# Kernel optimization log

Measured on AMD Instinct MI355X. Metric: run time of the kernel, lower is better.

The kernel has to match this reference:

```python
import jax, jax.numpy as jnp
import numpy as np

NUM_NODES = 200000
B = 65536          # n_id batch size
E = 131072         # events per direction
D_MEM = 128
D_RAW = 128
D_TIME = 128
T_MAX = 1000000


def setup_inputs() -> dict:
    key = jax.random.key(0)
    ks = jax.random.split(key, 16)
    inp = {
        'memory': jax.random.normal(ks[0], (NUM_NODES, D_MEM), jnp.float32),
        'last_update': jax.random.randint(ks[1], (NUM_NODES,), 0, 1000, jnp.int64),
        'n_id': jnp.arange(B, dtype=jnp.int64),
        'src_s': jax.random.randint(ks[2], (E,), 0, B, jnp.int64),
        'dst_s': jax.random.randint(ks[3], (E,), 0, B, jnp.int64),
        't_s': jax.random.randint(ks[4], (E,), 0, T_MAX, jnp.int64),
        'raw_msg_s': jax.random.normal(ks[5], (E, D_RAW), jnp.float32),
        'src_d': jax.random.randint(ks[6], (E,), 0, B, jnp.int64),
        'dst_d': jax.random.randint(ks[7], (E,), 0, B, jnp.int64),
        't_d': jax.random.randint(ks[8], (E,), 0, T_MAX, jnp.int64),
        'raw_msg_d': jax.random.normal(ks[9], (E, D_RAW), jnp.float32),
        'w_time': jax.random.normal(ks[10], (D_TIME, 1), jnp.float32) * 0.1,
        'b_time': jax.random.normal(ks[11], (D_TIME,), jnp.float32) * 0.1,
        'W_ih': jax.random.normal(ks[12], (3 * D_MEM, 2 * D_MEM + D_RAW + D_TIME), jnp.float32) * 0.05,
        'W_hh': jax.random.normal(ks[13], (3 * D_MEM, D_MEM), jnp.float32) * 0.05,
        'b_ih': jax.random.normal(ks[14], (3 * D_MEM,), jnp.float32) * 0.05,
        'b_hh': jax.random.normal(ks[15], (3 * D_MEM,), jnp.float32) * 0.05,
    }
    return inp


def _time_enc(t_rel, w_time, b_time):
    # Linear(1, time_dim) followed by cos: cos(t * w + b)
    return jnp.cos(t_rel.astype(jnp.float32)[:, None] * w_time[:, 0][None, :] + b_time)


def reference(memory, last_update, n_id, src_s, dst_s, t_s, raw_msg_s,
              src_d, dst_d, t_d, raw_msg_d, w_time, b_time, W_ih, W_hh, b_ih, b_hh):
    nb = n_id.shape[0]
    # assoc: global node id -> local index within n_id
    assoc = jnp.zeros((memory.shape[0],), dtype=jnp.int32).at[n_id].set(
        jnp.arange(nb, dtype=jnp.int32))

    # source-side messages (IdentityMessage = concat)
    t_enc_s = _time_enc(t_s - last_update[src_s], w_time, b_time)
    msg_s = jnp.concatenate([memory[src_s], memory[dst_s], raw_msg_s, t_enc_s], axis=-1)

    # destination-side messages
    t_enc_d = _time_enc(t_d - last_update[dst_d], w_time, b_time)
    msg_d = jnp.concatenate([memory[dst_d], memory[src_d], raw_msg_d, t_enc_d], axis=-1)

    idx = jnp.concatenate([src_s, dst_d], axis=0)       # [2E] global ids
    msg = jnp.concatenate([msg_s, msg_d], axis=0)       # [2E, 512]
    t = jnp.concatenate([t_s, t_d], axis=0)             # [2E]
    loc = assoc[idx]                                     # [2E] local ids

    # LastAggregator: per local node, pick the message with max t (ties -> latest position)
    ne = t.shape[0]
    key = t * ne + jnp.arange(ne, dtype=t.dtype)         # encode (t, position)
    maxkey = jax.ops.segment_max(key, loc, num_segments=nb)
    count = jax.ops.segment_sum(jnp.ones_like(loc), loc, num_segments=nb)
    has = count > 0
    argm = jnp.where(has, maxkey % ne, 0)
    aggr = jnp.where(has[:, None], msg[argm], 0.0)       # [nb, 512]

    # GRUCell(x=aggr, h=memory[n_id])
    h = memory[n_id]
    gi = aggr @ W_ih.T + b_ih
    gh = h @ W_hh.T + b_hh
    gi_r, gi_z, gi_n = jnp.split(gi, 3, axis=-1)
    gh_r, gh_z, gh_n = jnp.split(gh, 3, axis=-1)
    r = jax.nn.sigmoid(gi_r + gh_r)
    z = jax.nn.sigmoid(gi_z + gh_z)
    n = jnp.tanh(gi_n + r * gh_n)
    new_memory = (1.0 - z) * n + z * h

    new_last_update = last_update.at[idx].set(t)[n_id]
    return new_memory, new_last_update
```

## Files before the change

kernel.cpp:

```cpp
#include <hip/hip_runtime.h>
#include <math.h>

#define NB        65536
#define EV        131072
#define NE        (2*EV)
#define DM        128
#define NO2       512
#define BM        64
#define NST       20
#define THREADS   512

typedef float f32x4 __attribute__((ext_vector_type(4)));
typedef unsigned long long u64;

__device__ __forceinline__ float fcos_rev(float rev) {
    float r; asm("v_cos_f32 %0, %1" : "=v"(r) : "v"(rev)); return r;
}
__device__ __forceinline__ float fexp2(float x) {
    float r; asm("v_exp_f32 %0, %1" : "=v"(r) : "v"(x)); return r;
}
__device__ __forceinline__ float frcp(float x) {
    float r; asm("v_rcp_f32 %0, %1" : "=v"(r) : "v"(x)); return r;
}
__device__ __forceinline__ float fast_cos(float arg) {
    double rv = (double)arg * 0.15915494309189535;
    rv -= floor(rv);
    return fcos_rev((float)rv);
}
__device__ __forceinline__ float fsigmoid(float x) {
    x = fminf(fmaxf(x, -30.f), 30.f);
    float e = fexp2(-1.44269504088896f * x);
    return frcp(1.f + e);
}
__device__ __forceinline__ float ftanh_(float x) {
    x = fminf(fmaxf(x, -15.f), 15.f);
    float e = fexp2(-2.88539008177793f * x);
    return (1.f - e) * frcp(1.f + e);
}

#if defined(__has_builtin) && __has_builtin(__builtin_amdgcn_cvt_pk_fp8_f32)
__device__ __forceinline__ unsigned pack4_fp8(float f0, float f1, float f2, float f3) {
    int v = __builtin_amdgcn_cvt_pk_fp8_f32(f0, f1, 0, false);
    v = __builtin_amdgcn_cvt_pk_fp8_f32(f2, f3, v, true);
    return (unsigned)v;
}
#else
__device__ __forceinline__ unsigned enc1_fp8(float x) {
    unsigned u = __float_as_uint(x);
    unsigned s = (u >> 24) & 0x80u;
    float a = fabsf(x);
    if (!(a >= 0.001953125f)) return s;
    if (a > 448.f) a = 448.f;
    int e; float mf = frexpf(a, &e);
    int E = e + 6, mant;
    if (E <= 0) {
        mant = (int)(a * 512.f + 0.5f);
        if (mant > 7) return s | 0x08u;
        return s | (unsigned)mant;
    }
    mant = (int)((mf * 2.f - 1.f) * 8.f + 0.5f);
    if (mant == 8) { mant = 0; ++E; }
    if (E > 15) { E = 15; mant = 6; }
    if (E == 15 && mant == 7) mant = 6;
    return s | (unsigned)(E << 3) | (unsigned)mant;
}
__device__ __forceinline__ unsigned pack4_fp8(float f0, float f1, float f2, float f3) {
    return enc1_fp8(f0) | (enc1_fp8(f1) << 8) | (enc1_fp8(f2) << 16) | (enc1_fp8(f3) << 24);
}
#endif

__global__ void prep_k(const int* __restrict__ src_s, const int* __restrict__ t_s,
                       const int* __restrict__ dst_d, const int* __restrict__ t_d,
                       u64* __restrict__ keyarr, u64* __restrict__ lukey,
                       const float* __restrict__ W_ih, const float* __restrict__ W_hh,
                       const float* __restrict__ b_ih, const float* __restrict__ b_hh,
                       unsigned char* __restrict__ wp8, float* __restrict__ bp) {
    int bid = blockIdx.x;
    if (bid < NE / 256) {
        int e = bid * 256 + threadIdx.x;
        int g, t;
        if (e < EV) { g = src_s[e];      t = t_s[e]; }
        else        { g = dst_d[e - EV]; t = t_d[e - EV]; }
        u64 key = ((u64)(unsigned)t << 18) + (u64)(unsigned)e + 1ull;
        atomicMax(&keyarr[g], key);
        u64 lk = ((u64)(unsigned)(e + 1) << 20) | (u64)(unsigned)t;
        atomicMax(&lukey[g], lk);
        return;
    }
    int idx = (bid - NE / 256) * 256 + threadIdx.x;
    int col = idx / 80, g = idx - col * 80;
    int step = g >> 2, sl = g & 3;
    int kg = sl ^ ((col >> 2) & 3);
    int k0 = step * 32 + kg * 8;
    int d = col >> 2, gate = col & 3;
    float f[8];
    #pragma unroll
    for (int j = 0; j < 8; ++j) {
        int c = k0 + j;
        float v = 0.f;
        if (c < 512) {
            int row = (gate == 0) ? d : (gate == 1) ? 128 + d : (gate == 2) ? 256 + d : -1;
            if (row >= 0) v = W_ih[(size_t)row * 512 + c];
        } else {
            int ch = c - 512;
            int row = (gate == 0) ? d : (gate == 1) ? 128 + d : (gate == 3) ? 256 + d : -1;
            if (row >= 0) v = W_hh[(size_t)row * 128 + ch];
        }
        f[j] = v * 16.f;
    }
    unsigned lo = pack4_fp8(f[0], f[1], f[2], f[3]);
    unsigned hi = pack4_fp8(f[4], f[5], f[6], f[7]);
    *(u64*)(wp8 + (size_t)step * 16384 + (size_t)col * 32 + (size_t)sl * 8)
        = (u64)lo | ((u64)hi << 32);
    if (g == 0) {
        float bv = (gate == 0) ? b_ih[d] + b_hh[d]
                 : (gate == 1) ? b_ih[128 + d] + b_hh[128 + d]
                 : (gate == 2) ? b_ih[256 + d] : b_hh[256 + d];
        bp[col] = bv;
    }
}

__global__ __launch_bounds__(THREADS, 4) void gemm_gru_k(
    const float* __restrict__ memory, const int* __restrict__ last_update,
    const int* __restrict__ src_s, const int* __restrict__ dst_s,
    const int* __restrict__ t_s, const float* __restrict__ raw_s,
    const int* __restrict__ src_d, const int* __restrict__ dst_d,
    const int* __restrict__ t_d, const float* __restrict__ raw_d,
    const float* __restrict__ w_time, const float* __restrict__ b_time,
    const unsigned char* __restrict__ wp8, const float* __restrict__ bp,
    const u64* __restrict__ keyarr, const u64* __restrict__ lukey,
    float* __restrict__ out_mem, float* __restrict__ out_lu)
{
    __shared__ __align__(16) char smem[56320];
    unsigned char* sA = (unsigned char*)smem;
    unsigned char* sB = (unsigned char*)(smem + 6144);
    float* sW = (float*)(smem + 55296);
    float* sBt= (float*)(smem + 55808);

    const int tid = threadIdx.x;
    const int m0  = blockIdx.x * BM;
    const int ln  = tid & 63, wn = tid >> 6;
    const int l2  = ln >> 4, rl = ln & 15;

    if (tid < DM) { sW[tid] = w_time[tid]; sBt[tid] = b_time[tid]; }

    const int ar = tid >> 3, ac = tid & 7;
    const int m  = m0 + ar;
    const u64 kk = keyarr[m];
    const int rv = (kk != 0ull);
    int a_ = 0, b_ = 0, t_ = 0;
    const float* pR = raw_s;
    if (kk) {
        int e = (int)((kk - 1ull) & (u64)(NE - 1));
        if (e < EV) { a_ = src_s[e]; b_ = dst_s[e]; t_ = t_s[e]; pR = raw_s + (size_t)e * DM; }
        else { int e2 = e - EV; a_ = dst_d[e2]; b_ = src_d[e2]; t_ = t_d[e2]; pR = raw_d + (size_t)e2 * DM; }
    }
    const float rt = rv ? (float)(t_ - last_update[a_]) : 0.f;
    const float* pA = memory + (size_t)a_ * DM;
    const float* pB = memory + (size_t)b_ * DM;
    const float* pH = memory + (size_t)m  * DM;

    float4 pv;
    auto PREF_A = [&](int step) {
        int seg = step >> 2;
        if (seg == 3) return;
        const float* base = (seg == 0) ? pA : (seg == 1) ? pB : (seg == 2) ? pR : pH;
        pv = *(const float4*)(base + ((step & 3) << 5) + (ac << 2));
    };
    auto STAGE_B = [&](int step, int buf) {
        const unsigned char* src = wp8 + (size_t)step * 16384 + (size_t)tid * 16;
        unsigned char* dst = sB + (size_t)buf * 16384 + (size_t)tid * 16;
        __builtin_amdgcn_global_load_lds((const __attribute__((address_space(1))) void*)src,
            (__attribute__((address_space(3))) void*)dst, 16, 0, 0);
        __builtin_amdgcn_global_load_lds((const __attribute__((address_space(1))) void*)(src + 8192),
            (__attribute__((address_space(3))) void*)(dst + 8192), 16, 0, 0);
    };
    auto WRITE_A = [&](int step, int buf) {
        int seg = step >> 2;
        float f0, f1, f2, f3;
        if (seg == 3) {
            int coff = ((step & 3) << 5) + (ac << 2);
            f0 = fast_cos(__fadd_rn(__fmul_rn(rt, sW[coff+0]), sBt[coff+0]));
            f1 = fast_cos(__fadd_rn(__fmul_rn(rt, sW[coff+1]), sBt[coff+1]));
            f2 = fast_cos(__fadd_rn(__fmul_rn(rt, sW[coff+2]), sBt[coff+2]));
            f3 = fast_cos(__fadd_rn(__fmul_rn(rt, sW[coff+3]), sBt[coff+3]));
        } else {
            f0 = pv.x; f1 = pv.y; f2 = pv.z; f3 = pv.w;
        }
        if (seg < 4 && !rv) { f0 = f1 = f2 = f3 = 0.f; }
        unsigned q = pack4_fp8(f0, f1, f2, f3);
        *(unsigned*)(sA + buf * 2048 + ar * 32
                     + ((((ac >> 1) ^ ((ar >> 2) & 3)) << 3) + ((ac & 1) << 2))) = q;
    };

    long afr[4], bfr[4];
    auto READ_FRAGS = [&](int buf) {
        #pragma unroll
        for (int mf = 0; mf < 4; ++mf) {
            int r = mf * 16 + rl;
            afr[mf] = *(const long*)(sA + buf * 2048 + r * 32 + ((l2 ^ ((r >> 2) & 3)) << 3));
        }
        #pragma unroll
        for (int nf = 0; nf < 4; ++nf) {
            int c = wn * 64 + nf * 16 + rl;
            bfr[nf] = *(const long*)(sB + buf * 16384 + c * 32 + ((l2 ^ ((c >> 2) & 3)) << 3));
        }
    };

    f32x4 acc[4][4];
    #pragma unroll
    for (int mf = 0; mf < 4; ++mf)
        #pragma unroll
        for (int nf = 0; nf < 4; ++nf)
            acc[mf][nf] = (f32x4){0.f, 0.f, 0.f, 0.f};

    PREF_A(0);
    WRITE_A(0, 0);
    PREF_A(1);
    WRITE_A(1, 1);
    STAGE_B(0, 0);
    STAGE_B(1, 1);
    PREF_A(2);
    asm volatile("s_waitcnt vmcnt(1) lgkmcnt(0)" ::: "memory");
    __builtin_amdgcn_sched_barrier(0);
    __builtin_amdgcn_s_barrier();
    READ_FRAGS(0);
    asm volatile("s_waitcnt lgkmcnt(0)" ::: "memory");
    __builtin_amdgcn_sched_barrier(0);

    #pragma unroll
    for (int k = 0; k < NST; ++k) {
        __builtin_amdgcn_s_setprio(1);
        #pragma unroll
        for (int mf = 0; mf < 4; ++mf)
            #pragma unroll
            for (int nf = 0; nf < 4; ++nf)
                acc[mf][nf] = __builtin_amdgcn_mfma_f32_16x16x32_fp8_fp8(
                    afr[mf], bfr[nf], acc[mf][nf], 0, 0, 0);
        __builtin_amdgcn_s_setprio(0);
        __builtin_amdgcn_sched_barrier(0);

        if (k + 2 <= NST - 1) {
            WRITE_A(k + 2, (k + 2) % 3);
            __builtin_amdgcn_sched_barrier(0);
            STAGE_B(k + 2, (k + 2) % 3);
            __builtin_amdgcn_sched_barrier(0);
        }
        const bool pf = (k + 3 <= NST - 1) && (((k + 3) >> 2) != 3);
        if (pf) PREF_A(k + 3);
        __builtin_amdgcn_sched_barrier(0);

        if (k + 1 <= NST - 1) READ_FRAGS((k + 1) % 3);

        if (k < NST - 1) {
            __builtin_amdgcn_sched_barrier(0);
            if (pf) asm volatile("s_waitcnt vmcnt(1) lgkmcnt(0)" ::: "memory");
            else    asm volatile("s_waitcnt vmcnt(0) lgkmcnt(0)" ::: "memory");
            __builtin_amdgcn_sched_barrier(0);
            __builtin_amdgcn_s_barrier();
        }
    }

    if (tid < BM) {
        u64 lk = lukey[m0 + tid];
        out_lu[m0 + tid] = lk ? (float)(unsigned)(lk & 0xFFFFFull)
                              : (float)last_update[m0 + tid];
    }
    __syncthreads();

    float* ep = (float*)(smem + wn * 4352);
    const int row16 = ln >> 2, dgrp = ln & 3;
    const int dbase = wn * 16 + dgrp * 4;
    const float ds = 0.0625f;
    f32x4 bb0 = *(const f32x4*)(bp + (dbase + 0) * 4);
    f32x4 bb1 = *(const f32x4*)(bp + (dbase + 1) * 4);
    f32x4 bb2 = *(const f32x4*)(bp + (dbase + 2) * 4);
    f32x4 bb3 = *(const f32x4*)(bp + (dbase + 3) * 4);

    #pragma unroll
    for (int mf = 0; mf < 4; ++mf) {
        #pragma unroll
        for (int nf = 0; nf < 4; ++nf)
            #pragma unroll
            for (int j = 0; j < 4; ++j)
                ep[((ln >> 4) * 4 + j) * 68 + nf * 16 + rl] = acc[mf][nf][j] * ds;
        asm volatile("s_waitcnt lgkmcnt(0)" ::: "memory");

        const int gm = m0 + mf * 16 + row16;
        const float* gr = ep + row16 * 68 + dgrp * 16;
        f32x4 g0 = *(const f32x4*)(gr + 0);
        f32x4 g1 = *(const f32x4*)(gr + 4);
        f32x4 g2 = *(const f32x4*)(gr + 8);
        f32x4 g3 = *(const f32x4*)(gr + 12);
        f32x4 h  = *(const f32x4*)(memory + (size_t)gm * DM + dbase);
        f32x4 res;
        {
            float rg = fsigmoid(g0.x + bb0.x);
            float zg = fsigmoid(g0.y + bb0.y);
            float ng = ftanh_(g0.z + bb0.z + rg * (g0.w + bb0.w));
            res.x = (1.f - zg) * ng + zg * h.x;
        }
        {
            float rg = fsigmoid(g1.x + bb1.x);
            float zg = fsigmoid(g1.y + bb1.y);
            float ng = ftanh_(g1.z + bb1.z + rg * (g1.w + bb1.w));
            res.y = (1.f - zg) * ng + zg * h.y;
        }
        {
            float rg = fsigmoid(g2.x + bb2.x);
            float zg = fsigmoid(g2.y + bb2.y);
            float ng = ftanh_(g2.z + bb2.z + rg * (g2.w + bb2.w));
            res.z = (1.f - zg) * ng + zg * h.z;
        }
        {
            float rg = fsigmoid(g3.x + bb3.x);
            float zg = fsigmoid(g3.y + bb3.y);
            float ng = ftanh_(g3.z + bb3.z + rg * (g3.w + bb3.w));
            res.w = (1.f - zg) * ng + zg * h.w;
        }
        *(f32x4*)(out_mem + (size_t)gm * DM + dbase) = res;
        if (mf < 3) asm volatile("s_waitcnt lgkmcnt(0)" ::: "memory");
    }
}

extern "C" void kernel_launch(void* const* d_in, const int* in_sizes, int n_in,
                              void* d_out, int out_size, void* d_ws, size_t ws_size,
                              hipStream_t stream) {
    const float* memory      = (const float*)d_in[0];
    const int*   last_update = (const int*)d_in[1];
    const int*   src_s       = (const int*)d_in[3];
    const int*   dst_s       = (const int*)d_in[4];
    const int*   t_s         = (const int*)d_in[5];
    const float* raw_s       = (const float*)d_in[6];
    const int*   src_d       = (const int*)d_in[7];
    const int*   dst_d       = (const int*)d_in[8];
    const int*   t_d         = (const int*)d_in[9];
    const float* raw_d       = (const float*)d_in[10];
    const float* w_time      = (const float*)d_in[11];
    const float* b_time      = (const float*)d_in[12];
    const float* W_ih        = (const float*)d_in[13];
    const float* W_hh        = (const float*)d_in[14];
    const float* b_ih        = (const float*)d_in[15];
    const float* b_hh        = (const float*)d_in[16];

    char* ws = (char*)d_ws;
    u64* keyarr = (u64*)ws;
    u64* lukey  = (u64*)(ws + 524288);
    unsigned char* wp8 = (unsigned char*)(ws + 1048576);
    float* bp = (float*)(ws + 1376256);

    hipMemsetAsync(d_ws, 0, 1048576, stream);

    prep_k<<<NE / 256 + (NO2 * 80) / 256, 256, 0, stream>>>(
        src_s, t_s, dst_d, t_d, keyarr, lukey, W_ih, W_hh, b_ih, b_hh, wp8, bp);

    float* out_mem = (float*)d_out;
    float* out_lu  = out_mem + (size_t)NB * DM;
    gemm_gru_k<<<NB / BM, THREADS, 0, stream>>>(memory, last_update,
        src_s, dst_s, t_s, raw_s, src_d, dst_d, t_d, raw_d,
        w_time, b_time, wp8, bp, keyarr, lukey, out_mem, out_lu);
}
```

Before: 80.19 us.

## Switch GEMM to 32x32x64 scaled FP8 MFMA with B streamed from global

The fused gather-GEMM-GRU kernel now uses the MI355X scaled f8f6f4 32x32x64 MFMA in place of 16x16x32 FP8. Each block handles 32 rows with 256 threads and stages the whole 640-wide FP8 A tile into LDS in one pass; rows with no event gather from a zero page instead of being masked. B fragments are read straight from global/L2 in a new prepacked layout rather than staged through LDS. This drops the multi-stage LDS pipeline and most barriers, at the cost of every block re-reading the weights from cache and having less load/compute overlap.

New measurement: 90.52 us. +12.9%, slower.

```diff
diff --git a/kernel.cpp b/kernel.cpp
--- a/kernel.cpp
+++ b/kernel.cpp
@@ -6,11 +6,15 @@
 #define NE        (2*EV)
 #define DM        128
 #define NO2       512
-#define BM        64
-#define NST       20
-#define THREADS   512
-
-typedef float f32x4 __attribute__((ext_vector_type(4)));
+#define BMR       32
+#define NST       10
+#define THREADS   256
+#define ASTRIDE   656
+
+typedef float f32x4  __attribute__((ext_vector_type(4)));
+typedef float f32x16 __attribute__((ext_vector_type(16)));
+typedef int   i32x4  __attribute__((ext_vector_type(4)));
+typedef int   i32x8  __attribute__((ext_vector_type(8)));
 typedef unsigned long long u64;
 
 __device__ __forceinline__ float fcos_rev(float rev) {
@@ -88,10 +92,9 @@
         return;
     }
     int idx = (bid - NE / 256) * 256 + threadIdx.x;
-    int col = idx / 80, g = idx - col * 80;
-    int step = g >> 2, sl = g & 3;
-    int kg = sl ^ ((col >> 2) & 3);
-    int k0 = step * 32 + kg * 8;
+    int jq = idx & 3, l = (idx >> 2) & 63, ct = (idx >> 8) & 15, s = idx >> 12;
+    int col = ct * 32 + (l & 31);
+    int k0  = s * 64 + (l >> 5) * 32 + jq * 8;
     int d = col >> 2, gate = col & 3;
     float f[8];
     #pragma unroll
@@ -110,9 +113,9 @@
     }
     unsigned lo = pack4_fp8(f[0], f[1], f[2], f[3]);
     unsigned hi = pack4_fp8(f[4], f[5], f[6], f[7]);
-    *(u64*)(wp8 + (size_t)step * 16384 + (size_t)col * 32 + (size_t)sl * 8)
+    *(u64*)(wp8 + (size_t)s * 32768 + (size_t)ct * 2048 + (size_t)l * 32 + (size_t)jq * 8)
         = (u64)lo | ((u64)hi << 32);
-    if (g == 0) {
+    if (k0 == 0 && jq == 0) {
         float bv = (gate == 0) ? b_ih[d] + b_hh[d]
                  : (gate == 1) ? b_ih[128 + d] + b_hh[128 + d]
                  : (gate == 2) ? b_ih[256 + d] : b_hh[256 + d];
@@ -129,22 +132,18 @@
     const float* __restrict__ w_time, const float* __restrict__ b_time,
     const unsigned char* __restrict__ wp8, const float* __restrict__ bp,
     const u64* __restrict__ keyarr, const u64* __restrict__ lukey,
+    const float* __restrict__ zpage,
     float* __restrict__ out_mem, float* __restrict__ out_lu)
 {
-    __shared__ __align__(16) char smem[56320];
-    unsigned char* sA = (unsigned char*)smem;
-    unsigned char* sB = (unsigned char*)(smem + 6144);
-    float* sW = (float*)(smem + 55296);
-    float* sBt= (float*)(smem + 55808);
+    __shared__ __align__(16) char smem[37888];
+    unsigned char* A8 = (unsigned char*)smem;
 
     const int tid = threadIdx.x;
-    const int m0  = blockIdx.x * BM;
+    const int m0  = blockIdx.x * BMR;
     const int ln  = tid & 63, wn = tid >> 6;
-    const int l2  = ln >> 4, rl = ln & 15;
-
-    if (tid < DM) { sW[tid] = w_time[tid]; sBt[tid] = b_time[tid]; }
-
-    const int ar = tid >> 3, ac = tid & 7;
+    const int lg  = ln >> 5;
+
+    const int ar = tid >> 3, kc = tid & 7;
     const int m  = m0 + ar;
     const u64 kk = keyarr[m];
     const int rv = (kk != 0ull);
@@ -156,143 +155,128 @@
         else { int e2 = e - EV; a_ = dst_d[e2]; b_ = src_d[e2]; t_ = t_d[e2]; pR = raw_d + (size_t)e2 * DM; }
     }
     const float rt = rv ? (float)(t_ - last_update[a_]) : 0.f;
-    const float* pA = memory + (size_t)a_ * DM;
-    const float* pB = memory + (size_t)b_ * DM;
-    const float* pH = memory + (size_t)m  * DM;
-
-    float4 pv;
-    auto PREF_A = [&](int step) {
-        int seg = step >> 2;
-        if (seg == 3) return;
-        const float* base = (seg == 0) ? pA : (seg == 1) ? pB : (seg == 2) ? pR : pH;
-        pv = *(const float4*)(base + ((step & 3) << 5) + (ac << 2));
-    };
-    auto STAGE_B = [&](int step, int buf) {
-        const unsigned char* src = wp8 + (size_t)step * 16384 + (size_t)tid * 16;
-        unsigned char* dst = sB + (size_t)buf * 16384 + (size_t)tid * 16;
-        __builtin_amdgcn_global_load_lds((const __attribute__((address_space(1))) void*)src,
-            (__attribute__((address_space(3))) void*)dst, 16, 0, 0);
-        __builtin_amdgcn_global_load_lds((const __attribute__((address_space(1))) void*)(src + 8192),
-            (__attribute__((address_space(3))) void*)(dst + 8192), 16, 0, 0);
-    };
-    auto WRITE_A = [&](int step, int buf) {
-        int seg = step >> 2;
-        float f0, f1, f2, f3;
-        if (seg == 3) {
-            int coff = ((step & 3) << 5) + (ac << 2);
-            f0 = fast_cos(__fadd_rn(__fmul_rn(rt, sW[coff+0]), sBt[coff+0]));
-            f1 = fast_cos(__fadd_rn(__fmul_rn(rt, sW[coff+1]), sBt[coff+1]));
-            f2 = fast_cos(__fadd_rn(__fmul_rn(rt, sW[coff+2]), sBt[coff+2]));
-            f3 = fast_cos(__fadd_rn(__fmul_rn(rt, sW[coff+3]), sBt[coff+3]));
-        } else {
-            f0 = pv.x; f1 = pv.y; f2 = pv.z; f3 = pv.w;
-        }
-        if (seg < 4 && !rv) { f0 = f1 = f2 = f3 = 0.f; }
-        unsigned q = pack4_fp8(f0, f1, f2, f3);
-        *(unsigned*)(sA + buf * 2048 + ar * 32
-                     + ((((ac >> 1) ^ ((ar >> 2) & 3)) << 3) + ((ac & 1) << 2))) = q;
-    };
-
-    long afr[4], bfr[4];
-    auto READ_FRAGS = [&](int buf) {
-        #pragma unroll
-        for (int mf = 0; mf < 4; ++mf) {
-            int r = mf * 16 + rl;
-            afr[mf] = *(const long*)(sA + buf * 2048 + r * 32 + ((l2 ^ ((r >> 2) & 3)) << 3));
-        }
+    const float* pA = rv ? memory + (size_t)a_ * DM : zpage;
+    const float* pB = rv ? memory + (size_t)b_ * DM : zpage;
+    if (!rv) pR = zpage;
+    const float* pH = memory + (size_t)m * DM;
+
+    const int kf = kc * 16;
+    float4 q0[4], q1[4], q2[4], q4[4];
+    #pragma unroll
+    for (int i = 0; i < 4; ++i) q0[i] = *(const float4*)(pA + kf + i * 4);
+    #pragma unroll
+    for (int i = 0; i < 4; ++i) q1[i] = *(const float4*)(pB + kf + i * 4);
+    #pragma unroll
+    for (int i = 0; i < 4; ++i) q2[i] = *(const float4*)(pR + kf + i * 4);
+    #pragma unroll
+    for (int i = 0; i < 4; ++i) q4[i] = *(const float4*)(pH + kf + i * 4);
+    float4 wt[4], bt[4];
+    #pragma unroll
+    for (int i = 0; i < 4; ++i) wt[i] = *(const float4*)(w_time + kf + i * 4);
+    #pragma unroll
+    for (int i = 0; i < 4; ++i) bt[i] = *(const float4*)(b_time + kf + i * 4);
+
+    unsigned char* arow = A8 + ar * ASTRIDE + kc * 16;
+    {
+        i32x4 v;
+        #pragma unroll
+        for (int i = 0; i < 4; ++i) {
+            float c0 = rv ? fast_cos(__fadd_rn(__fmul_rn(rt, wt[i].x), bt[i].x)) : 0.f;
+            float c1 = rv ? fast_cos(__fadd_rn(__fmul_rn(rt, wt[i].y), bt[i].y)) : 0.f;
+            float c2 = rv ? fast_cos(__fadd_rn(__fmul_rn(rt, wt[i].z), bt[i].z)) : 0.f;
+            float c3 = rv ? fast_cos(__fadd_rn(__fmul_rn(rt, wt[i].w), bt[i].w)) : 0.f;
+            v[i] = (int)pack4_fp8(c0, c1, c2, c3);
+        }
+        *(i32x4*)(arow + 3 * 128) = v;
+    }
+    {   i32x4 v;
+        #pragma unroll
+        for (int i = 0; i < 4; ++i) v[i] = (int)pack4_fp8(q0[i].x, q0[i].y, q0[i].z, q0[i].w);
+        *(i32x4*)(arow + 0 * 128) = v; }
+    {   i32x4 v;
+        #pragma unroll
+        for (int i = 0; i < 4; ++i) v[i] = (int)pack4_fp8(q1[i].x, q1[i].y, q1[i].z, q1[i].w);
+        *(i32x4*)(arow + 1 * 128) = v; }
+    {   i32x4 v;
+        #pragma unroll
+        for (int i = 0; i < 4; ++i) v[i] = (int)pack4_fp8(q2[i].x, q2[i].y, q2[i].z, q2[i].w);
+        *(i32x4*)(arow + 2 * 128) = v; }
+    {   i32x4 v;
+        #pragma unroll
+        for (int i = 0; i < 4; ++i) v[i] = (int)pack4_fp8(q4[i].x, q4[i].y, q4[i].z, q4[i].w);
+        *(i32x4*)(arow + 4 * 128) = v; }
+
+    const unsigned char* bptr[4];
+    #pragma unroll
+    for (int nf = 0; nf < 4; ++nf)
+        bptr[nf] = wp8 + (size_t)(wn * 4 + nf) * 2048 + (size_t)ln * 32;
+
+    i32x8 b[4];
+    #pragma unroll
+    for (int nf = 0; nf < 4; ++nf) {
+        i32x4 lo = *(const i32x4*)(bptr[nf]);
+        i32x4 hi = *(const i32x4*)(bptr[nf] + 16);
+        b[nf] = (i32x8){lo.x,lo.y,lo.z,lo.w, hi.x,hi.y,hi.z,hi.w};
+    }
+
+    f32x16 acc[4];
+    #pragma unroll
+    for (int nf = 0; nf < 4; ++nf)
+        #pragma unroll
+        for (int j = 0; j < 16; ++j) acc[nf][j] = 0.f;
+
+    __syncthreads();
+
+    const unsigned char* arowf = A8 + (ln & 31) * ASTRIDE + lg * 32;
+    #pragma unroll
+    for (int k = 0; k < NST; ++k) {
+        i32x4 alo = *(const i32x4*)(arowf + k * 64);
+        i32x4 ahi = *(const i32x4*)(arowf + k * 64 + 16);
+        i32x8 af = (i32x8){alo.x,alo.y,alo.z,alo.w, ahi.x,ahi.y,ahi.z,ahi.w};
+
         #pragma unroll
         for (int nf = 0; nf < 4; ++nf) {
-            int c = wn * 64 + nf * 16 + rl;
-            bfr[nf] = *(const long*)(sB + buf * 16384 + c * 32 + ((l2 ^ ((c >> 2) & 3)) << 3));
-        }
-    };
-
-    f32x4 acc[4][4];
-    #pragma unroll
-    for (int mf = 0; mf < 4; ++mf)
-        #pragma unroll
-        for (int nf = 0; nf < 4; ++nf)
-            acc[mf][nf] = (f32x4){0.f, 0.f, 0.f, 0.f};
-
-    PREF_A(0);
-    WRITE_A(0, 0);
-    PREF_A(1);
-    WRITE_A(1, 1);
-    STAGE_B(0, 0);
-    STAGE_B(1, 1);
-    PREF_A(2);
-    asm volatile("s_waitcnt vmcnt(1) lgkmcnt(0)" ::: "memory");
-    __builtin_amdgcn_sched_barrier(0);
-    __builtin_amdgcn_s_barrier();
-    READ_FRAGS(0);
-    asm volatile("s_waitcnt lgkmcnt(0)" ::: "memory");
-    __builtin_amdgcn_sched_barrier(0);
-
-    #pragma unroll
-    for (int k = 0; k < NST; ++k) {
-        __builtin_amdgcn_s_setprio(1);
-        #pragma unroll
-        for (int mf = 0; mf < 4; ++mf)
-            #pragma unroll
-            for (int nf = 0; nf < 4; ++nf)
-                acc[mf][nf] = __builtin_amdgcn_mfma_f32_16x16x32_fp8_fp8(
-                    afr[mf], bfr[nf], acc[mf][nf], 0, 0, 0);
-        __builtin_amdgcn_s_setprio(0);
-        __builtin_amdgcn_sched_barrier(0);
-
-        if (k + 2 <= NST - 1) {
-            WRITE_A(k + 2, (k + 2) % 3);
-            __builtin_amdgcn_sched_barrier(0);
-            STAGE_B(k + 2, (k + 2) % 3);
-            __builtin_amdgcn_sched_barrier(0);
-        }
-        const bool pf = (k + 3 <= NST - 1) && (((k + 3) >> 2) != 3);
-        if (pf) PREF_A(k + 3);
-        __builtin_amdgcn_sched_barrier(0);
-
-        if (k + 1 <= NST - 1) READ_FRAGS((k + 1) % 3);
-
-        if (k < NST - 1) {
-            __builtin_amdgcn_sched_barrier(0);
-            if (pf) asm volatile("s_waitcnt vmcnt(1) lgkmcnt(0)" ::: "memory");
-            else    asm volatile("s_waitcnt vmcnt(0) lgkmcnt(0)" ::: "memory");
-            __builtin_amdgcn_sched_barrier(0);
-            __builtin_amdgcn_s_barrier();
-        }
-    }
-
-    if (tid < BM) {
+            acc[nf] = __builtin_amdgcn_mfma_scale_f32_32x32x64_f8f6f4(
+                af, b[nf], acc[nf], 0, 0, 0, 127, 0, 127);
+            if (k < NST - 1) {
+                i32x4 lo = *(const i32x4*)(bptr[nf] + (size_t)(k + 1) * 32768);
+                i32x4 hi = *(const i32x4*)(bptr[nf] + (size_t)(k + 1) * 32768 + 16);
+                b[nf] = (i32x8){lo.x,lo.y,lo.z,lo.w, hi.x,hi.y,hi.z,hi.w};
+            }
+        }
+    }
+
+    if (tid < BMR) {
         u64 lk = lukey[m0 + tid];
         out_lu[m0 + tid] = lk ? (float)(unsigned)(lk & 0xFFFFFull)
                               : (float)last_update[m0 + tid];
     }
-    __syncthreads();
-
-    float* ep = (float*)(smem + wn * 4352);
-    const int row16 = ln >> 2, dgrp = ln & 3;
-    const int dbase = wn * 16 + dgrp * 4;
+
+    float* ep = (float*)(smem + 20992 + wn * 4224);
+    const int erow = ln >> 1, half = ln & 1;
     const float ds = 0.0625f;
-    f32x4 bb0 = *(const f32x4*)(bp + (dbase + 0) * 4);
-    f32x4 bb1 = *(const f32x4*)(bp + (dbase + 1) * 4);
-    f32x4 bb2 = *(const f32x4*)(bp + (dbase + 2) * 4);
-    f32x4 bb3 = *(const f32x4*)(bp + (dbase + 3) * 4);
-
-    #pragma unroll
-    for (int mf = 0; mf < 4; ++mf) {
-        #pragma unroll
-        for (int nf = 0; nf < 4; ++nf)
-            #pragma unroll
-            for (int j = 0; j < 4; ++j)
-                ep[((ln >> 4) * 4 + j) * 68 + nf * 16 + rl] = acc[mf][nf][j] * ds;
+
+    #pragma unroll
+    for (int nf = 0; nf < 4; ++nf) {
+        #pragma unroll
+        for (int reg = 0; reg < 16; ++reg) {
+            int r32 = (reg & 3) + 8 * (reg >> 2) + 4 * lg;
+            ep[r32 * 33 + (ln & 31)] = acc[nf][reg] * ds;
+        }
         asm volatile("s_waitcnt lgkmcnt(0)" ::: "memory");
 
-        const int gm = m0 + mf * 16 + row16;
-        const float* gr = ep + row16 * 68 + dgrp * 16;
+        const int gm = m0 + erow;
+        const int dbase = wn * 32 + nf * 8 + half * 4;
+        const float* gr = ep + erow * 33 + half * 16;
         f32x4 g0 = *(const f32x4*)(gr + 0);
         f32x4 g1 = *(const f32x4*)(gr + 4);
         f32x4 g2 = *(const f32x4*)(gr + 8);
         f32x4 g3 = *(const f32x4*)(gr + 12);
-        f32x4 h  = *(const f32x4*)(memory + (size_t)gm * DM + dbase);
+        f32x4 bb0 = *(const f32x4*)(bp + (dbase + 0) * 4);
+        f32x4 bb1 = *(const f32x4*)(bp + (dbase + 1) * 4);
+        f32x4 bb2 = *(const f32x4*)(bp + (dbase + 2) * 4);
+        f32x4 bb3 = *(const f32x4*)(bp + (dbase + 3) * 4);
+        f32x4 h = *(const f32x4*)(memory + (size_t)gm * DM + dbase);
         f32x4 res;
         {
             float rg = fsigmoid(g0.x + bb0.x);
@@ -319,7 +303,7 @@
             res.w = (1.f - zg) * ng + zg * h.w;
         }
         *(f32x4*)(out_mem + (size_t)gm * DM + dbase) = res;
-        if (mf < 3) asm volatile("s_waitcnt lgkmcnt(0)" ::: "memory");
+        asm volatile("s_waitcnt lgkmcnt(0)" ::: "memory");
     }
 }
 
@@ -346,17 +330,18 @@
     char* ws = (char*)d_ws;
     u64* keyarr = (u64*)ws;
     u64* lukey  = (u64*)(ws + 524288);
-    unsigned char* wp8 = (unsigned char*)(ws + 1048576);
-    float* bp = (float*)(ws + 1376256);
-
-    hipMemsetAsync(d_ws, 0, 1048576, stream);
-
-    prep_k<<<NE / 256 + (NO2 * 80) / 256, 256, 0, stream>>>(
+    float* zpage = (float*)(ws + 1048576);
+    unsigned char* wp8 = (unsigned char*)(ws + 1049088);
+    float* bp = (float*)(ws + 1376768);
+
+    hipMemsetAsync(d_ws, 0, 1049088, stream);
+
+    prep_k<<<NE / 256 + 160, 256, 0, stream>>>(
         src_s, t_s, dst_d, t_d, keyarr, lukey, W_ih, W_hh, b_ih, b_hh, wp8, bp);
 
     float* out_mem = (float*)d_out;
     float* out_lu  = out_mem + (size_t)NB * DM;
-    gemm_gru_k<<<NB / BM, THREADS, 0, stream>>>(memory, last_update,
+    gemm_gru_k<<<NB / BMR, THREADS, 0, stream>>>(memory, last_update,
         src_s, dst_s, t_s, raw_s, src_d, dst_d, t_d, raw_d,
-        w_time, b_time, wp8, bp, keyarr, lukey, out_mem, out_lu);
-}
+        w_time, b_time, wp8, bp, keyarr, lukey, zpage, out_mem, out_lu);
+}
```
